# Performance work log

Measured on AMD Instinct MI355X. Metric: run time of the kernel, lower is better.

Reference implementation:

```python
import jax, jax.numpy as jnp
import numpy as np

N, NF, INF, NHID = 8192, 128, 128, 16


def _gcn(x, adj, dis, W, b):
    # GraphConvolution: support = x @ W; aggregate with distance-weighted adjacency
    support = x @ W  # [N, out]
    return (adj * dis) @ support + b


def setup_inputs() -> dict:
    key = jax.random.key(0)
    ks = jax.random.split(key, 26)

    def lin(k, i, o):
        kw, kb = jax.random.split(k)
        W = jax.random.uniform(kw, (i, o), jnp.float32, -1.0, 1.0) / np.sqrt(i).astype(np.float32)
        b = jax.random.uniform(kb, (o,), jnp.float32, -1.0, 1.0) / np.sqrt(i).astype(np.float32)
        return W, b

    x = jax.random.normal(ks[0], (N, NF), jnp.float32)
    adj = jax.random.uniform(ks[1], (N, N), jnp.float32)
    dis = jax.random.uniform(ks[2], (N, N), jnp.float32)

    W1, b1 = lin(ks[3], NF, NF)        # linear1
    Wg1, bg1 = lin(ks[4], NF, INF)     # gc1
    Wm1, bm1 = lin(ks[5], INF, 64)     # linear_med1
    Wm2, bm2 = lin(ks[6], 64, 128)     # linear_med2
    Wm3, bm3 = lin(ks[7], 128, 64)     # linear_med3
    Wm4, bm4 = lin(ks[8], 64, 64)      # linear_med4
    Wgh, bgh = lin(ks[9], 64, 64)      # gconv_hidden[0]
    W2, b2 = lin(ks[10], 64, 32)       # linear2
    Wg2, bg2 = lin(ks[11], 32, 32)     # gc2
    W3, b3 = lin(ks[12], 32, NHID)     # linear3

    return dict(x=x, adj=adj, dis=dis, W1=W1, b1=b1, Wg1=Wg1, bg1=bg1,
                Wm1=Wm1, bm1=bm1, Wm2=Wm2, bm2=bm2, Wm3=Wm3, bm3=bm3,
                Wm4=Wm4, bm4=bm4, Wgh=Wgh, bgh=bgh, W2=W2, b2=b2,
                Wg2=Wg2, bg2=bg2, W3=W3, b3=b3)


def reference(x, adj, dis, W1, b1, Wg1, bg1, Wm1, bm1, Wm2, bm2, Wm3, bm3,
              Wm4, bm4, Wgh, bgh, W2, b2, Wg2, bg2, W3, b3):
    lrelu = lambda v: jax.nn.leaky_relu(v, 0.2)
    x0 = _gcn(x @ W1 + b1, adj, dis, Wg1, bg1)
    x0 = lrelu(x0 @ Wm1 + bm1)
    x0 = lrelu(x0 @ Wm2 + bm2)
    x0 = lrelu(x0 @ Wm3 + bm3)
    x0 = jax.nn.relu(x0 @ Wm4 + bm4)
    x_res = x0
    x0 = jax.nn.relu(_gcn(x0, adj, dis, Wgh, bgh) + x_res)  # one hidden gconv layer
    x0 = x0 @ W2 + b2
    x0 = _gcn(x0, adj, dis, Wg2, bg2)
    return x0 @ W3 + b3
```

## Files before the change

kernel.cpp:

```cpp
#include <hip/hip_runtime.h>
#include <hip/hip_bf16.h>

#define NROWS 8192
typedef unsigned short u16;
typedef short bf16x8 __attribute__((ext_vector_type(8)));
typedef float f32x4 __attribute__((ext_vector_type(4)));

__device__ __forceinline__ u16 f2b(float f) {
    unsigned u = __float_as_uint(f);
    unsigned r = (u + 0x7fffu + ((u >> 16) & 1u)) >> 16;
    return (u16)r;
}

template<int MODE> __device__ __forceinline__ float actf(float v) {
    if constexpr (MODE == 1) return fmaxf(v, 0.f);
    else if constexpr (MODE == 2) return v > 0.f ? v : 0.2f * v;
    else return v;
}

__global__ __launch_bounds__(256) void fold1(
    const float* __restrict__ W1, const float* __restrict__ b1,
    const float* __restrict__ Wg1,
    const float* __restrict__ W2, const float* __restrict__ b2,
    const float* __restrict__ Wg2, float* __restrict__ ws) {
    float* T2 = ws + 9376;
    float* v1 = ws + 11424;
    float* v2 = ws + 11552;
    float* T1 = ws + 16384;
    const int tid = threadIdx.x, b = blockIdx.x;
    if (b < 16) {
        int i = b * 8 + (tid >> 5), j4 = (tid & 31) << 2;
        float4 acc = {0, 0, 0, 0};
        for (int k = 0; k < 128; ++k) {
            float a = W1[i * 128 + k];
            float4 g = *(const float4*)&Wg1[k * 128 + j4];
            acc.x += a * g.x; acc.y += a * g.y; acc.z += a * g.z; acc.w += a * g.w;
        }
        *(float4*)&T1[i * 128 + j4] = acc;
    } else if (b == 16) {
        if (tid < 128) {
            float s = 0;
            for (int k = 0; k < 128; ++k) s += b1[k] * Wg1[k * 128 + tid];
            v1[tid] = s;
        } else if (tid < 160) {
            int j = tid - 128;
            float s = 0;
            for (int k = 0; k < 32; ++k) s += b2[k] * Wg2[k * 32 + j];
            v2[j] = s;
        }
    } else {
        for (int o4 = tid; o4 < 64 * 8; o4 += 256) {
            int i = o4 >> 3, j4 = (o4 & 7) << 2;
            float4 acc = {0, 0, 0, 0};
            for (int k = 0; k < 32; ++k) {
                float a = W2[i * 32 + k];
                float4 g = *(const float4*)&Wg2[k * 32 + j4];
                acc.x += a * g.x; acc.y += a * g.y; acc.z += a * g.z; acc.w += a * g.w;
            }
            *(float4*)&T2[i * 32 + j4] = acc;
        }
    }
}

__global__ __launch_bounds__(256) void fold2(
    const float* __restrict__ Wm1, const float* __restrict__ bm1,
    const float* __restrict__ bg1,
    const float* __restrict__ W3, const float* __restrict__ b3,
    const float* __restrict__ bg2, float* __restrict__ ws) {
    float* WA = ws + 0;
    float* bA = ws + 8192;
    float* cA = ws + 8256;
    float* WB = ws + 8320;
    float* bB = ws + 9344;
    float* cB = ws + 9360;
    const float* T2 = ws + 9376;
    const float* v1 = ws + 11424;
    const float* v2 = ws + 11552;
    const float* T1 = ws + 16384;
    const int tid = threadIdx.x, b = blockIdx.x;
    if (b < 8) {
        int i = b * 16 + (tid >> 4), j4 = (tid & 15) << 2;
        float4 acc = {0, 0, 0, 0};
        for (int k = 0; k < 128; ++k) {
            float a = T1[i * 128 + k];
            float4 g = *(const float4*)&Wm1[k * 64 + j4];
            acc.x += a * g.x; acc.y += a * g.y; acc.z += a * g.z; acc.w += a * g.w;
        }
        *(float4*)&WA[i * 64 + j4] = acc;
    } else if (b == 8) {
        if (tid < 64) {
            float s = 0, c = 0;
            for (int k = 0; k < 128; ++k) {
                s += v1[k] * Wm1[k * 64 + tid];
                c += bg1[k] * Wm1[k * 64 + tid];
            }
            bA[tid] = s; cA[tid] = c + bm1[tid];
        } else if (tid < 80) {
            int j = tid - 64;
            float s = 0, c = 0;
            for (int k = 0; k < 32; ++k) {
                s += v2[k] * W3[k * 16 + j];
                c += bg2[k] * W3[k * 16 + j];
            }
            bB[j] = s; cB[j] = c + b3[j];
        }
    } else {
        int i = tid >> 2, j4 = (tid & 3) << 2;
        float4 acc = {0, 0, 0, 0};
        for (int k = 0; k < 32; ++k) {
            float a = T2[i * 32 + k];
            float4 g = *(const float4*)&W3[k * 16 + j4];
            acc.x += a * g.x; acc.y += a * g.y; acc.z += a * g.z; acc.w += a * g.w;
        }
        *(float4*)&WB[i * 16 + j4] = acc;
    }
}

template<int K, int M, int AIN, int AOUT, int OUTT>
__global__ __launch_bounds__(256) void gemm_rows(
    const float* __restrict__ in, const float* __restrict__ W,
    const float* __restrict__ bias, void* __restrict__ outv) {
    constexpr int RB = 32;
    constexpr int TNs = (M >= 64) ? 4 : 2;
    constexpr int TXs = M / TNs;
    constexpr int TYs = 256 / TXs;
    constexpr int TMs = RB / TYs;
    static_assert(TMs >= 1 && TMs * TYs == RB, "bad cfg");
    __shared__ float in_t[K][RB + 4];
    __shared__ float w_s[K * M];
    __shared__ float bias_s[M];
    const int tid = threadIdx.x;
    const int b0 = blockIdx.x * RB;
    constexpr int K4 = K / 4;
    for (int g = tid; g < RB * K4; g += 256) {
        int r = g / K4, c4 = g % K4;
        float4 v = *(const float4*)&in[(size_t)(b0 + r) * K + c4 * 4];
        v.x = actf<AIN>(v.x); v.y = actf<AIN>(v.y);
        v.z = actf<AIN>(v.z); v.w = actf<AIN>(v.w);
        in_t[c4 * 4 + 0][r] = v.x;
        in_t[c4 * 4 + 1][r] = v.y;
        in_t[c4 * 4 + 2][r] = v.z;
        in_t[c4 * 4 + 3][r] = v.w;
    }
    for (int g = tid; g < K * M / 4; g += 256)
        ((float4*)w_s)[g] = ((const float4*)W)[g];
    if (tid < M) bias_s[tid] = bias ? bias[tid] : 0.f;
    __syncthreads();

    const int tx = tid % TXs, ty = tid / TXs;
    const int c0 = tx * TNs, r0 = ty * TMs;
    float acc[TMs][TNs] = {};
    for (int k = 0; k < K; ++k) {
        float a[TMs];
#pragma unroll
        for (int m = 0; m < TMs; ++m) a[m] = in_t[k][r0 + m];
        float w[TNs];
#pragma unroll
        for (int n = 0; n < TNs; ++n) w[n] = w_s[k * M + c0 + n];
#pragma unroll
        for (int m = 0; m < TMs; ++m)
#pragma unroll
            for (int n = 0; n < TNs; ++n) acc[m][n] += a[m] * w[n];
    }
#pragma unroll
    for (int m = 0; m < TMs; ++m) {
        float vres[TNs];
#pragma unroll
        for (int n = 0; n < TNs; ++n) vres[n] = actf<AOUT>(acc[m][n] + bias_s[c0 + n]);
        if constexpr (OUTT == 0) {
            float* op = &((float*)outv)[(size_t)(b0 + r0 + m) * M + c0];
            if constexpr (TNs == 4) { float4 o4 = {vres[0], vres[1], vres[2], vres[3]}; *(float4*)op = o4; }
            else                    { float2 o2 = {vres[0], vres[1]}; *(float2*)op = o2; }
        } else {
            u16* ot = (u16*)outv;
#pragma unroll
            for (int n = 0; n < TNs; ++n)
                ot[(size_t)(c0 + n) * NROWS + (b0 + r0 + m)] = f2b(vres[n]);
        }
    }
}

template<int F, int MODE, int KS>
__global__ __launch_bounds__(256) void agg_mfma(
    u16* __restrict__ Abf, const float* __restrict__ adj,
    const float* __restrict__ dis, const u16* __restrict__ St,
    float* __restrict__ Pout) {
    constexpr int CT = F / 16;
    constexpr int KCH = NROWS / KS;
    const int lane = threadIdx.x & 63;
    const int wid  = threadIdx.x >> 6;
    const int r0   = blockIdx.x * 64 + wid * 16;
    const int ky   = blockIdx.y;
    const int l15  = lane & 15;
    const int kb   = (lane >> 4) * 8;
    const int k0   = ky * KCH;
    f32x4 acc[CT] = {};
    size_t aoff = (size_t)(r0 + l15) * NROWS + k0 + kb;
    const u16* Bbase = St + (size_t)l15 * NROWS + k0 + kb;
#pragma unroll 4
    for (int ks = 0; ks < KCH; ks += 32) {
        bf16x8 af;
        if constexpr (MODE == 0) {
            af = *(const bf16x8*)(Abf + aoff);
        } else {
            const f32x4* a4 = (const f32x4*)(adj + aoff);
            const f32x4* d4 = (const f32x4*)(dis + aoff);
            f32x4 a0 = __builtin_nontemporal_load(a4);
            f32x4 a1 = __builtin_nontemporal_load(a4 + 1);
            f32x4 d0 = __builtin_nontemporal_load(d4);
            f32x4 d1 = __builtin_nontemporal_load(d4 + 1);
#pragma unroll
            for (int j = 0; j < 4; ++j) {
                af[j]     = (short)f2b(a0[j] * d0[j]);
                af[j + 4] = (short)f2b(a1[j] * d1[j]);
            }
            if constexpr (MODE == 1)
                *(bf16x8*)(Abf + aoff) = af;
        }
#pragma unroll
        for (int ct = 0; ct < CT; ++ct) {
            bf16x8 bf = *(const bf16x8*)(Bbase + (size_t)ct * 16 * NROWS + ks);
            acc[ct] = __builtin_amdgcn_mfma_f32_16x16x32_bf16(af, bf, acc[ct], 0, 0, 0);
        }
        aoff += 32;
    }
    float* P = Pout + (size_t)ky * ((size_t)NROWS * F);
    const int rb = r0 + (lane >> 4) * 4;
#pragma unroll
    for (int ct = 0; ct < CT; ++ct)
#pragma unroll
        for (int i = 0; i < 4; ++i)
            P[(size_t)(rb + i) * F + ct * 16 + l15] = acc[ct][i];
}

template<int F, int KS>
__global__ __launch_bounds__(256) void reduce_add(
    const float* __restrict__ P, const float* __restrict__ bias,
    const float* __restrict__ res, float* __restrict__ out) {
    constexpr int TOT4 = NROWS * F / 4;
    int i = blockIdx.x * 256 + threadIdx.x;
    if (i >= TOT4) return;
    constexpr size_t STR = (size_t)NROWS * F / 4;
    const float4* P4 = (const float4*)P;
    float4 s = P4[i];
#pragma unroll
    for (int k = 1; k < KS; ++k) {
        float4 t = P4[i + (size_t)k * STR];
        s.x += t.x; s.y += t.y; s.z += t.z; s.w += t.w;
    }
    float4 b = *(const float4*)&bias[(i % (F / 4)) * 4];
    s.x += b.x; s.y += b.y; s.z += b.z; s.w += b.w;
    if (res) {
        float4 r = ((const float4*)res)[i];
        s.x += r.x; s.y += r.y; s.z += r.z; s.w += r.w;
    }
    ((float4*)out)[i] = s;
}

extern "C" void kernel_launch(void* const* d_in, const int* in_sizes, int n_in,
                              void* d_out, int out_size, void* d_ws, size_t ws_size,
                              hipStream_t stream) {
    const float* x   = (const float*)d_in[0];
    const float* adj = (const float*)d_in[1];
    const float* dis = (const float*)d_in[2];
    const float* W1  = (const float*)d_in[3];
    const float* b1  = (const float*)d_in[4];
    const float* Wg1 = (const float*)d_in[5];
    const float* bg1 = (const float*)d_in[6];
    const float* Wm1 = (const float*)d_in[7];
    const float* bm1 = (const float*)d_in[8];
    const float* Wm2 = (const float*)d_in[9];
    const float* bm2 = (const float*)d_in[10];
    const float* Wm3 = (const float*)d_in[11];
    const float* bm3 = (const float*)d_in[12];
    const float* Wm4 = (const float*)d_in[13];
    const float* bm4 = (const float*)d_in[14];
    const float* Wgh = (const float*)d_in[15];
    const float* bgh = (const float*)d_in[16];
    const float* W2  = (const float*)d_in[17];
    const float* b2  = (const float*)d_in[18];
    const float* Wg2 = (const float*)d_in[19];
    const float* bg2 = (const float*)d_in[20];
    const float* W3  = (const float*)d_in[21];
    const float* b3  = (const float*)d_in[22];
    float* ws  = (float*)d_ws;
    float* out = (float*)d_out;

    constexpr int KS = 8;
    const size_t ABF_FLOATS = (size_t)NROWS * NROWS / 2;
    const size_t BASE_FLOATS = 40960 + 262144 + (size_t)KS * 524288 + 524288 + 524288;
    const size_t NEED_PRE_BYTES = (ABF_FLOATS + BASE_FLOATS) * 4ULL;
    const bool pre = ws_size >= NEED_PRE_BYTES;

    float* base = ws + (pre ? ABF_FLOATS : 0);
    float* wsW  = base;
    float* St_f = wsW + 40960;
    float* P    = St_f + 262144;
    float* h2   = P;
    float* h3   = P + 1048576;
    float* gA   = P + (size_t)KS * 524288;
    float* h4   = gA + 524288;
    float* g2   = gA;

    u16* Abf = (u16*)ws;
    u16* St  = (u16*)St_f;
    const float* WA = wsW + 0;
    const float* bA = wsW + 8192;
    const float* cA = wsW + 8256;
    const float* WB = wsW + 8320;
    const float* bB = wsW + 9344;
    const float* cB = wsW + 9360;

    fold1<<<18, 256, 0, stream>>>(W1, b1, Wg1, W2, b2, Wg2, wsW);
    fold2<<<10, 256, 0, stream>>>(Wm1, bm1, bg1, W3, b3, bg2, wsW);

    gemm_rows<128, 64, 0, 0, 1><<<256, 256, 0, stream>>>(x, WA, bA, St);
    if (pre) agg_mfma<64, 1, KS><<<dim3(128, KS), 256, 0, stream>>>(Abf, adj, dis, St, P);
    else     agg_mfma<64, 2, KS><<<dim3(128, KS), 256, 0, stream>>>(nullptr, adj, dis, St, P);
    reduce_add<64, KS><<<512, 256, 0, stream>>>(P, cA, nullptr, gA);

    gemm_rows<64, 128, 2, 2, 0><<<256, 256, 0, stream>>>(gA, Wm2, bm2, h2);
    gemm_rows<128, 64, 0, 2, 0><<<256, 256, 0, stream>>>(h2, Wm3, bm3, h3);
    gemm_rows<64, 64, 0, 1, 0><<<256, 256, 0, stream>>>(h3, Wm4, bm4, h4);

    gemm_rows<64, 64, 0, 0, 1><<<256, 256, 0, stream>>>(h4, Wgh, nullptr, St);
    if (pre) agg_mfma<64, 0, KS><<<dim3(128, KS), 256, 0, stream>>>(Abf, nullptr, nullptr, St, P);
    else     agg_mfma<64, 2, KS><<<dim3(128, KS), 256, 0, stream>>>(nullptr, adj, dis, St, P);
    reduce_add<64, KS><<<512, 256, 0, stream>>>(P, bgh, h4, g2);

    gemm_rows<64, 16, 1, 0, 1><<<256, 256, 0, stream>>>(g2, WB, bB, St);
    if (pre) agg_mfma<16, 0, KS><<<dim3(128, KS), 256, 0, stream>>>(Abf, nullptr, nullptr, St, P);
    else     agg_mfma<16, 2, KS><<<dim3(128, KS), 256, 0, stream>>>(nullptr, adj, dis, St, P);
    reduce_add<16, KS><<<128, 256, 0, stream>>>(P, cB, nullptr, out);
}
```

Measured before the change: 370.1 us.

## Fuse middle MLP layers into one kernel and software-pipeline aggregation loads

Replaces four separate gemm_rows launches (Wm2, Wm3, Wm4, Wgh) with a single med_chain kernel. It keeps 32-row activation tiles and weights in shared memory across layers, which removes the global round-trips of the h2/h3 intermediates and three launches. Separately, the agg_mfma inner loop is rewritten as a two-stage double-buffered pipeline that issues the loads for the next iterations before running the MFMAs of the current ones, to hide memory latency. The cost is higher register and shared-memory use (about 90KB LDS per block), which may reduce occupancy.

Result: slower. 406.9 us (+10.0%).

```diff
diff --git a/kernel.cpp b/kernel.cpp
--- a/kernel.cpp
+++ b/kernel.cpp
@@ -180,6 +180,120 @@
     }
 }
 
+template<int K, int M, int AOUT, int OMODE>
+__device__ __forceinline__ void layer_step(
+    const float (*pin)[33], const float* w, const float* bias,
+    float (*pout)[33], float* gout, u16* stout, int b0, int tid) {
+    constexpr int TXs = M / 4;
+    constexpr int TYs = 256 / TXs;
+    constexpr int TMs = 32 / TYs;
+    const int tx = tid % TXs, ty = tid / TXs;
+    const int c0 = tx * 4, r0 = ty * TMs;
+    float acc[TMs][4] = {};
+    for (int k = 0; k < K; ++k) {
+        float4 wv = *(const float4*)&w[k * M + c0];
+#pragma unroll
+        for (int m = 0; m < TMs; ++m) {
+            float a = pin[k][r0 + m];
+            acc[m][0] += a * wv.x; acc[m][1] += a * wv.y;
+            acc[m][2] += a * wv.z; acc[m][3] += a * wv.w;
+        }
+    }
+#pragma unroll
+    for (int m = 0; m < TMs; ++m) {
+        float v[4];
+#pragma unroll
+        for (int n = 0; n < 4; ++n) {
+            float bv = bias ? bias[c0 + n] : 0.f;
+            v[n] = actf<AOUT>(acc[m][n] + bv);
+        }
+        if constexpr (OMODE != 2) {
+#pragma unroll
+            for (int n = 0; n < 4; ++n) pout[c0 + n][r0 + m] = v[n];
+        }
+        if constexpr (OMODE == 1) {
+            float4 o = {v[0], v[1], v[2], v[3]};
+            *(float4*)&gout[(size_t)(b0 + r0 + m) * M + c0] = o;
+        }
+        if constexpr (OMODE == 2) {
+#pragma unroll
+            for (int n = 0; n < 4; ++n)
+                stout[(size_t)(c0 + n) * NROWS + (b0 + r0 + m)] = f2b(v[n]);
+        }
+    }
+}
+
+__global__ __launch_bounds__(256) void med_chain(
+    const float* __restrict__ gA,
+    const float* __restrict__ Wm2, const float* __restrict__ bm2,
+    const float* __restrict__ Wm3, const float* __restrict__ bm3,
+    const float* __restrict__ Wm4, const float* __restrict__ bm4,
+    const float* __restrict__ Wgh,
+    float* __restrict__ h4, u16* __restrict__ St) {
+    __shared__ __align__(16) float P0[64][33];
+    __shared__ __align__(16) float P1[128][33];
+    __shared__ __align__(16) float P2[64][33];
+    __shared__ __align__(16) float wb0[8192];
+    __shared__ __align__(16) float wb1[8192];
+    __shared__ float bias128[128], bias64a[64], bias64b[64];
+    const int tid = threadIdx.x;
+    const int b0 = blockIdx.x * 32;
+
+    for (int g = tid; g < 32 * 16; g += 256) {
+        int r = g >> 4, c4 = g & 15;
+        float4 v = *(const float4*)&gA[(size_t)(b0 + r) * 64 + c4 * 4];
+        P0[c4 * 4 + 0][r] = actf<2>(v.x);
+        P0[c4 * 4 + 1][r] = actf<2>(v.y);
+        P0[c4 * 4 + 2][r] = actf<2>(v.z);
+        P0[c4 * 4 + 3][r] = actf<2>(v.w);
+    }
+    for (int g = tid; g < 2048; g += 256) ((float4*)wb0)[g] = ((const float4*)Wm2)[g];
+    for (int g = tid; g < 2048; g += 256) ((float4*)wb1)[g] = ((const float4*)Wm3)[g];
+    if (tid < 128) bias128[tid] = bm2[tid];
+    else if (tid < 192) bias64a[tid - 128] = bm3[tid - 128];
+    else bias64b[tid - 192] = bm4[tid - 192];
+    __syncthreads();
+    layer_step<64, 128, 2, 0>(P0, wb0, bias128, P1, nullptr, nullptr, b0, tid);
+    __syncthreads();
+    for (int g = tid; g < 1024; g += 256) ((float4*)wb0)[g] = ((const float4*)Wm4)[g];
+    for (int g = tid; g < 1024; g += 256) ((float4*)(wb0 + 4096))[g] = ((const float4*)Wgh)[g];
+    layer_step<128, 64, 2, 0>(P1, wb1, bias64a, P2, nullptr, nullptr, b0, tid);
+    __syncthreads();
+    layer_step<64, 64, 1, 1>(P2, wb0, bias64b, P0, h4, nullptr, b0, tid);
+    __syncthreads();
+    layer_step<64, 64, 0, 2>(P0, wb0 + 4096, nullptr, nullptr, nullptr, St, b0, tid);
+}
+
+#define AGG_ISSUE(S, T) { \
+    size_t ao_ = aoff + (size_t)(T) * 32; \
+    if constexpr (MODE == 0) { raf##S = *(const bf16x8*)(Abf + ao_); } \
+    else { \
+        const f32x4* a4_ = (const f32x4*)(adj + ao_); \
+        const f32x4* d4_ = (const f32x4*)(dis + ao_); \
+        a0##S = __builtin_nontemporal_load(a4_); \
+        a1##S = __builtin_nontemporal_load(a4_ + 1); \
+        d0##S = __builtin_nontemporal_load(d4_); \
+        d1##S = __builtin_nontemporal_load(d4_ + 1); \
+    } \
+    const u16* bB_ = Bbase + (size_t)(T) * 32; \
+    _Pragma("unroll") \
+    for (int ct = 0; ct < CT; ++ct) rb##S[ct] = *(const bf16x8*)(bB_ + (size_t)ct * 16 * NROWS); }
+
+#define AGG_STEP(S, T) { \
+    bf16x8 af_; \
+    if constexpr (MODE == 0) { af_ = raf##S; } \
+    else { \
+        _Pragma("unroll") \
+        for (int j = 0; j < 4; ++j) { \
+            af_[j]     = (short)f2b(a0##S[j] * d0##S[j]); \
+            af_[j + 4] = (short)f2b(a1##S[j] * d1##S[j]); \
+        } \
+        if constexpr (MODE == 1) *(bf16x8*)(Abf + aoff + (size_t)(T) * 32) = af_; \
+    } \
+    _Pragma("unroll") \
+    for (int ct = 0; ct < CT; ++ct) \
+        acc[ct] = __builtin_amdgcn_mfma_f32_16x16x32_bf16(af_, rb##S[ct], acc[ct], 0, 0, 0); }
+
 template<int F, int MODE, int KS>
 __global__ __launch_bounds__(256) void agg_mfma(
     u16* __restrict__ Abf, const float* __restrict__ adj,
@@ -187,6 +301,8 @@
     float* __restrict__ Pout) {
     constexpr int CT = F / 16;
     constexpr int KCH = NROWS / KS;
+    constexpr int NIT = KCH / 32;
+    static_assert(NIT >= 4 && (NIT & 1) == 0, "pipeline needs even NIT>=4");
     const int lane = threadIdx.x & 63;
     const int wid  = threadIdx.x >> 6;
     const int r0   = blockIdx.x * 64 + wid * 16;
@@ -197,33 +313,22 @@
     f32x4 acc[CT] = {};
     size_t aoff = (size_t)(r0 + l15) * NROWS + k0 + kb;
     const u16* Bbase = St + (size_t)l15 * NROWS + k0 + kb;
-#pragma unroll 4
-    for (int ks = 0; ks < KCH; ks += 32) {
-        bf16x8 af;
-        if constexpr (MODE == 0) {
-            af = *(const bf16x8*)(Abf + aoff);
-        } else {
-            const f32x4* a4 = (const f32x4*)(adj + aoff);
-            const f32x4* d4 = (const f32x4*)(dis + aoff);
-            f32x4 a0 = __builtin_nontemporal_load(a4);
-            f32x4 a1 = __builtin_nontemporal_load(a4 + 1);
-            f32x4 d0 = __builtin_nontemporal_load(d4);
-            f32x4 d1 = __builtin_nontemporal_load(d4 + 1);
-#pragma unroll
-            for (int j = 0; j < 4; ++j) {
-                af[j]     = (short)f2b(a0[j] * d0[j]);
-                af[j + 4] = (short)f2b(a1[j] * d1[j]);
-            }
-            if constexpr (MODE == 1)
-                *(bf16x8*)(Abf + aoff) = af;
-        }
-#pragma unroll
-        for (int ct = 0; ct < CT; ++ct) {
-            bf16x8 bf = *(const bf16x8*)(Bbase + (size_t)ct * 16 * NROWS + ks);
-            acc[ct] = __builtin_amdgcn_mfma_f32_16x16x32_bf16(af, bf, acc[ct], 0, 0, 0);
-        }
-        aoff += 32;
-    }
+
+    f32x4 a0A, a1A, d0A, d1A, a0B, a1B, d0B, d1B;
+    bf16x8 rafA, rafB;
+    bf16x8 rbA[CT], rbB[CT];
+
+    AGG_ISSUE(A, 0)
+    AGG_ISSUE(B, 1)
+    for (int t = 0; t < NIT - 2; t += 2) {
+        AGG_STEP(A, t)
+        AGG_ISSUE(A, t + 2)
+        AGG_STEP(B, t + 1)
+        AGG_ISSUE(B, t + 3)
+    }
+    AGG_STEP(A, NIT - 2)
+    AGG_STEP(B, NIT - 1)
+
     float* P = Pout + (size_t)ky * ((size_t)NROWS * F);
     const int rb = r0 + (lane >> 4) * 4;
 #pragma unroll
@@ -296,8 +401,6 @@
     float* wsW  = base;
     float* St_f = wsW + 40960;
     float* P    = St_f + 262144;
-    float* h2   = P;
-    float* h3   = P + 1048576;
     float* gA   = P + (size_t)KS * 524288;
     float* h4   = gA + 524288;
     float* g2   = gA;
@@ -319,11 +422,8 @@
     else     agg_mfma<64, 2, KS><<<dim3(128, KS), 256, 0, stream>>>(nullptr, adj, dis, St, P);
     reduce_add<64, KS><<<512, 256, 0, stream>>>(P, cA, nullptr, gA);
 
-    gemm_rows<64, 128, 2, 2, 0><<<256, 256, 0, stream>>>(gA, Wm2, bm2, h2);
-    gemm_rows<128, 64, 0, 2, 0><<<256, 256, 0, stream>>>(h2, Wm3, bm3, h3);
-    gemm_rows<64, 64, 0, 1, 0><<<256, 256, 0, stream>>>(h3, Wm4, bm4, h4);
-
-    gemm_rows<64, 64, 0, 0, 1><<<256, 256, 0, stream>>>(h4, Wgh, nullptr, St);
+    med_chain<<<256, 256, 0, stream>>>(gA, Wm2, bm2, Wm3, bm3, Wm4, bm4, Wgh, h4, St);
+
     if (pre) agg_mfma<64, 0, KS><<<dim3(128, KS), 256, 0, stream>>>(Abf, nullptr, nullptr, St, P);
     else     agg_mfma<64, 2, KS><<<dim3(128, KS), 256, 0, stream>>>(nullptr, adj, dis, St, P);
     reduce_add<64, KS><<<512, 256, 0, stream>>>(P, bgh, h4, g2);
```

## Fuse MLP chain into one kernel, store split-K partials as bf16, double split-K

Applied to the files above, without the earlier changes.

Replaces four separate gemm_rows launches for the linear_med2..4 and gconv_hidden support GEMMs with one med_chain kernel. It keeps 16-row tiles in shared memory between layers and writes h4 plus the bf16 transposed support directly. The split-K partial buffers in agg_mfma are now stored as bf16 instead of fp32, halving partial-sum traffic, and split-K goes from 8 to 16 to give the aggregation more parallelism. Rounding partials to bf16 before the reduction adds numerical error, and the extra split slices mean more partials to reduce.

Result: slower. 444.9 us (+20.2%).

```diff
diff --git a/kernel.cpp b/kernel.cpp
--- a/kernel.cpp
+++ b/kernel.cpp
@@ -10,6 +10,9 @@
     unsigned u = __float_as_uint(f);
     unsigned r = (u + 0x7fffu + ((u >> 16) & 1u)) >> 16;
     return (u16)r;
+}
+__device__ __forceinline__ float b2f(u16 v) {
+    return __uint_as_float(((unsigned)v) << 16);
 }
 
 template<int MODE> __device__ __forceinline__ float actf(float v) {
@@ -180,11 +183,88 @@
     }
 }
 
+template<int K, int M, int AOUT, int OMODE>
+__device__ __forceinline__ void layer_step(
+    const float (*pin)[17], const float* __restrict__ w,
+    const float* __restrict__ bias,
+    float (*pout)[17], float* __restrict__ gout, u16* __restrict__ stout,
+    int b0, int tid) {
+    constexpr int TXs = M / 4;
+    constexpr int TYs = 256 / TXs;
+    constexpr int TMs = 16 / TYs;
+    static_assert(TMs >= 1, "cfg");
+    const int tx = tid % TXs, ty = tid / TXs;
+    const int c0 = tx * 4, r0 = ty * TMs;
+    float acc[TMs][4] = {};
+    for (int k = 0; k < K; ++k) {
+        float4 wv = *(const float4*)&w[k * M + c0];
+#pragma unroll
+        for (int m = 0; m < TMs; ++m) {
+            float a = pin[k][r0 + m];
+            acc[m][0] += a * wv.x; acc[m][1] += a * wv.y;
+            acc[m][2] += a * wv.z; acc[m][3] += a * wv.w;
+        }
+    }
+#pragma unroll
+    for (int m = 0; m < TMs; ++m) {
+        float v[4];
+#pragma unroll
+        for (int n = 0; n < 4; ++n) {
+            float bv = bias ? bias[c0 + n] : 0.f;
+            v[n] = actf<AOUT>(acc[m][n] + bv);
+        }
+        if constexpr (OMODE != 2) {
+#pragma unroll
+            for (int n = 0; n < 4; ++n) pout[c0 + n][r0 + m] = v[n];
+        }
+        if constexpr (OMODE == 1) {
+            float4 o = {v[0], v[1], v[2], v[3]};
+            *(float4*)&gout[(size_t)(b0 + r0 + m) * M + c0] = o;
+        }
+        if constexpr (OMODE == 2) {
+#pragma unroll
+            for (int n = 0; n < 4; ++n)
+                stout[(size_t)(c0 + n) * NROWS + (b0 + r0 + m)] = f2b(v[n]);
+        }
+    }
+}
+
+__global__ __launch_bounds__(256) void med_chain(
+    const float* __restrict__ gA,
+    const float* __restrict__ Wm2, const float* __restrict__ bm2,
+    const float* __restrict__ Wm3, const float* __restrict__ bm3,
+    const float* __restrict__ Wm4, const float* __restrict__ bm4,
+    const float* __restrict__ Wgh,
+    float* __restrict__ h4, u16* __restrict__ St) {
+    __shared__ __align__(16) float P0[64][17];
+    __shared__ __align__(16) float P1[128][17];
+    __shared__ __align__(16) float P2[64][17];
+    const int tid = threadIdx.x;
+    const int b0 = blockIdx.x * 16;
+
+    {
+        int r = tid >> 4, c4 = tid & 15;
+        float4 v = *(const float4*)&gA[(size_t)(b0 + r) * 64 + c4 * 4];
+        P0[c4 * 4 + 0][r] = actf<2>(v.x);
+        P0[c4 * 4 + 1][r] = actf<2>(v.y);
+        P0[c4 * 4 + 2][r] = actf<2>(v.z);
+        P0[c4 * 4 + 3][r] = actf<2>(v.w);
+    }
+    __syncthreads();
+    layer_step<64, 128, 2, 0>(P0, Wm2, bm2, P1, nullptr, nullptr, b0, tid);
+    __syncthreads();
+    layer_step<128, 64, 2, 0>(P1, Wm3, bm3, P2, nullptr, nullptr, b0, tid);
+    __syncthreads();
+    layer_step<64, 64, 1, 1>(P2, Wm4, bm4, P0, h4, nullptr, b0, tid);
+    __syncthreads();
+    layer_step<64, 64, 0, 2>(P0, Wgh, nullptr, nullptr, nullptr, St, b0, tid);
+}
+
 template<int F, int MODE, int KS>
 __global__ __launch_bounds__(256) void agg_mfma(
     u16* __restrict__ Abf, const float* __restrict__ adj,
     const float* __restrict__ dis, const u16* __restrict__ St,
-    float* __restrict__ Pout) {
+    u16* __restrict__ Pout) {
     constexpr int CT = F / 16;
     constexpr int KCH = NROWS / KS;
     const int lane = threadIdx.x & 63;
@@ -224,37 +304,42 @@
         }
         aoff += 32;
     }
-    float* P = Pout + (size_t)ky * ((size_t)NROWS * F);
+    u16* P = Pout + (size_t)ky * ((size_t)NROWS * F);
     const int rb = r0 + (lane >> 4) * 4;
 #pragma unroll
     for (int ct = 0; ct < CT; ++ct)
 #pragma unroll
         for (int i = 0; i < 4; ++i)
-            P[(size_t)(rb + i) * F + ct * 16 + l15] = acc[ct][i];
+            P[(size_t)(rb + i) * F + ct * 16 + l15] = f2b(acc[ct][i]);
 }
 
 template<int F, int KS>
 __global__ __launch_bounds__(256) void reduce_add(
-    const float* __restrict__ P, const float* __restrict__ bias,
+    const u16* __restrict__ P, const float* __restrict__ bias,
     const float* __restrict__ res, float* __restrict__ out) {
-    constexpr int TOT4 = NROWS * F / 4;
-    int i = blockIdx.x * 256 + threadIdx.x;
-    if (i >= TOT4) return;
-    constexpr size_t STR = (size_t)NROWS * F / 4;
-    const float4* P4 = (const float4*)P;
-    float4 s = P4[i];
-#pragma unroll
-    for (int k = 1; k < KS; ++k) {
-        float4 t = P4[i + (size_t)k * STR];
-        s.x += t.x; s.y += t.y; s.z += t.z; s.w += t.w;
-    }
-    float4 b = *(const float4*)&bias[(i % (F / 4)) * 4];
-    s.x += b.x; s.y += b.y; s.z += b.z; s.w += b.w;
+    constexpr int TOT8 = NROWS * F / 8;
+    int i8 = blockIdx.x * 256 + threadIdx.x;
+    if (i8 >= TOT8) return;
+    constexpr size_t STR = (size_t)NROWS * F;
+    float s[8] = {};
+#pragma unroll
+    for (int k = 0; k < KS; ++k) {
+        bf16x8 v = *(const bf16x8*)(P + (size_t)k * STR + (size_t)i8 * 8);
+#pragma unroll
+        for (int j = 0; j < 8; ++j) s[j] += b2f((u16)v[j]);
+    }
+    const int c0 = (i8 * 8) % F;
+#pragma unroll
+    for (int j = 0; j < 8; ++j) s[j] += bias[c0 + j];
     if (res) {
-        float4 r = ((const float4*)res)[i];
-        s.x += r.x; s.y += r.y; s.z += r.z; s.w += r.w;
-    }
-    ((float4*)out)[i] = s;
+        const float4* r4 = (const float4*)(res + (size_t)i8 * 8);
+        float4 ra = r4[0], rb = r4[1];
+        s[0] += ra.x; s[1] += ra.y; s[2] += ra.z; s[3] += ra.w;
+        s[4] += rb.x; s[5] += rb.y; s[6] += rb.z; s[7] += rb.w;
+    }
+    float4* o4 = (float4*)(out + (size_t)i8 * 8);
+    float4 oa = {s[0], s[1], s[2], s[3]}, ob = {s[4], s[5], s[6], s[7]};
+    o4[0] = oa; o4[1] = ob;
 }
 
 extern "C" void kernel_launch(void* const* d_in, const int* in_sizes, int n_in,
@@ -286,24 +371,24 @@
     float* ws  = (float*)d_ws;
     float* out = (float*)d_out;
 
-    constexpr int KS = 8;
+    constexpr int KS = 16;
     const size_t ABF_FLOATS = (size_t)NROWS * NROWS / 2;
-    const size_t BASE_FLOATS = 40960 + 262144 + (size_t)KS * 524288 + 524288 + 524288;
+    const size_t P_FLOATS = (size_t)KS * NROWS * 64 / 2;
+    const size_t BASE_FLOATS = 40960 + 262144 + P_FLOATS + 524288 + 524288;
     const size_t NEED_PRE_BYTES = (ABF_FLOATS + BASE_FLOATS) * 4ULL;
     const bool pre = ws_size >= NEED_PRE_BYTES;
 
     float* base = ws + (pre ? ABF_FLOATS : 0);
     float* wsW  = base;
     float* St_f = wsW + 40960;
-    float* P    = St_f + 262144;
-    float* h2   = P;
-    float* h3   = P + 1048576;
-    float* gA   = P + (size_t)KS * 524288;
+    float* P_f  = St_f + 262144;
+    float* gA   = P_f + P_FLOATS;
     float* h4   = gA + 524288;
     float* g2   = gA;
 
     u16* Abf = (u16*)ws;
     u16* St  = (u16*)St_f;
+    u16* P   = (u16*)P_f;
     const float* WA = wsW + 0;
     const float* bA = wsW + 8192;
     const float* cA = wsW + 8256;
@@ -317,19 +402,16 @@
     gemm_rows<128, 64, 0, 0, 1><<<256, 256, 0, stream>>>(x, WA, bA, St);
     if (pre) agg_mfma<64, 1, KS><<<dim3(128, KS), 256, 0, stream>>>(Abf, adj, dis, St, P);
     else     agg_mfma<64, 2, KS><<<dim3(128, KS), 256, 0, stream>>>(nullptr, adj, dis, St, P);
-    reduce_add<64, KS><<<512, 256, 0, stream>>>(P, cA, nullptr, gA);
-
-    gemm_rows<64, 128, 2, 2, 0><<<256, 256, 0, stream>>>(gA, Wm2, bm2, h2);
-    gemm_rows<128, 64, 0, 2, 0><<<256, 256, 0, stream>>>(h2, Wm3, bm3, h3);
-    gemm_rows<64, 64, 0, 1, 0><<<256, 256, 0, stream>>>(h3, Wm4, bm4, h4);
-
-    gemm_rows<64, 64, 0, 0, 1><<<256, 256, 0, stream>>>(h4, Wgh, nullptr, St);
+    reduce_add<64, KS><<<256, 256, 0, stream>>>(P, cA, nullptr, gA);
+
+    med_chain<<<512, 256, 0, stream>>>(gA, Wm2, bm2, Wm3, bm3, Wm4, bm4, Wgh, h4, St);
+
     if (pre) agg_mfma<64, 0, KS><<<dim3(128, KS), 256, 0, stream>>>(Abf, nullptr, nullptr, St, P);
     else     agg_mfma<64, 2, KS><<<dim3(128, KS), 256, 0, stream>>>(nullptr, adj, dis, St, P);
-    reduce_add<64, KS><<<512, 256, 0, stream>>>(P, bgh, h4, g2);
+    reduce_add<64, KS><<<256, 256, 0, stream>>>(P, bgh, h4, g2);
 
     gemm_rows<64, 16, 1, 0, 1><<<256, 256, 0, stream>>>(g2, WB, bB, St);
     if (pre) agg_mfma<16, 0, KS><<<dim3(128, KS), 256, 0, stream>>>(Abf, nullptr, nullptr, St, P);
     else     agg_mfma<16, 2, KS><<<dim3(128, KS), 256, 0, stream>>>(nullptr, adj, dis, St, P);
-    reduce_add<16, KS><<<128, 256, 0, stream>>>(P, cB, nullptr, out);
-}
+    reduce_add<16, KS><<<64, 256, 0, stream>>>(P, cB, nullptr, out);
+}
```
